# Kernel tuning notes

Hardware: AMD Instinct MI355X
Metric: run time of the kernel (lower is better)

The kernel has to match this reference:

```python
import jax, jax.numpy as jnp
import numpy as np

LK = 8  # db4 has 8 taps
LEVEL = 5
# pywt.Wavelet('db4').filter_bank[0] == dec_lo
DB4_LO = np.array([-0.010597401784997278, 0.032883011666982945, 0.030841381835986965,
                   -0.18703481171888114, -0.02798376941698385, 0.6308807679295904,
                   0.7148465705525415, 0.23037781330885523], dtype=np.float32)
DN = ('NCH', 'OIH', 'NCH')


def _wpt_kernels(level):
    # Filter_Free WPT: distinct kernel per child node; parent j even -> (lp, hp), odd -> (hp, lp)
    cmf = (-1.0) ** np.arange(LK)
    k_lp = DB4_LO
    k_hp = (DB4_LO[::-1] * cmf).astype(np.float32)
    ks = []
    for i in range(level):
        rows = []
        for j in range(2 ** i):
            rows += [k_lp, k_hp] if j % 2 == 0 else [k_hp, k_lp]
        ks.append(jnp.asarray(np.stack(rows)))  # [2^(i+1), LK]
    return ks


def setup_inputs() -> dict:
    key = jax.random.key(0)
    kx, kb = jax.random.split(key)
    B, N = 128, 32768
    inp = {'x': jax.random.normal(kx, (B, 1, N), dtype=jnp.float32)}
    for i, K in enumerate(_wpt_kernels(LEVEL)):
        inp[f'k{i + 1}'] = K
    for i in range(LEVEL):
        kb, sub = jax.random.split(kb)
        # small positive thresholds (Act_Init=0 would make the threshold an exact identity)
        inp[f'b{i + 1}'] = 0.1 * jax.random.uniform(sub, (2 ** (i + 1),), dtype=jnp.float32)
    return inp


def _analysis(c, K, b):
    # c: [B, G, M] parents -> [B, 2G, M//2] children; one grouped 8-tap conv for the whole level
    G = c.shape[1]
    cp = jnp.pad(c, ((0, 0), (0, 0), (LK // 2 - 1, LK // 2)))
    y = jax.lax.conv_general_dilated(cp, K[:, None, :], (2,), 'VALID',
                                     feature_group_count=G, dimension_numbers=DN)
    bb = b[None, :, None]
    # symmetric sigmoid soft-threshold (Thresh_SigSym), fused elementwise
    return y * (jax.nn.sigmoid(10.0 * (y - bb)) + jax.nn.sigmoid(-10.0 * (y + bb)))


def _synthesis(y, K):
    # adjoint of the strided analysis conv (conv_transpose): [B, 2G, M] -> [B, G, 2M]
    G = y.shape[1] // 2
    M = y.shape[2]
    W = jnp.flip(K, -1).reshape(G, 2, LK)  # sum the two children of each parent
    out = jax.lax.conv_general_dilated(y, W, (1,), [(LK - 1, LK - 1)], lhs_dilation=(2,),
                                       feature_group_count=G, dimension_numbers=DN)
    pl = LK // 2 - 1  # undo analysis left pad
    return out[:, :, pl:pl + 2 * M]


def reference(x, k1, k2, k3, k4, k5, b1, b2, b3, b4, b5):
    Ks = [k1, k2, k3, k4, k5]
    bs = [b1, b2, b3, b4, b5]
    c = x  # [B, 1, N]
    for K, b in zip(Ks, bs):
        c = _analysis(c, K, b)
    for K in Ks[::-1]:
        c = _synthesis(c, K)
    return c  # [B, 1, N] reconstruction
```

## Files before the change

### kernel.cpp

```cpp
#include <hip/hip_runtime.h>

#define TPB 256

constexpr int NSEQ = 32768;
constexpr int C0   = 2048;


__device__ __forceinline__ float gate(float y, float bb) {
    float e1 = __expf(-10.f * (y - bb));
    float e2 = __expf( 10.f * (y + bb));
    return __builtin_amdgcn_rcpf(1.f + e1) + __builtin_amdgcn_rcpf(1.f + e2);
}

template<int Sin, int Sout, int P, int Gout, int Nlev>
__device__ __forceinline__ void analysis_r4(
    const float* __restrict__ in, float* __restrict__ out,
    const float* __restrict__ kf, const float* __restrict__ bias, int outBase)
{
    constexpr int TPC = P / 4;
    constexpr int TOT = (Gout / 2) * TPC;
    for (int task = threadIdx.x; task < TOT; task += TPB) {
        const int c  = task / TPC;
        const int i0 = (task - c * TPC) * 4;

        float w[16];
        {
            const float4* ip = reinterpret_cast<const float4*>(in + c * Sin + 2 * i0);
            reinterpret_cast<float4*>(w)[0] = ip[0];
            reinterpret_cast<float4*>(w)[1] = ip[1];
            reinterpret_cast<float4*>(w)[2] = ip[2];
            reinterpret_cast<float4*>(w)[3] = ip[3];
        }
        float k0[8], k1[8];
        {
            const float4* kp = reinterpret_cast<const float4*>(kf + (2 * c) * 8);
            reinterpret_cast<float4*>(k0)[0] = kp[0];
            reinterpret_cast<float4*>(k0)[1] = kp[1];
            reinterpret_cast<float4*>(k1)[0] = kp[2];
            reinterpret_cast<float4*>(k1)[1] = kp[3];
        }
        const float b0 = bias[2 * c];
        const float b1 = bias[2 * c + 1];

        float o0[4], o1[4];
#pragma unroll
        for (int r = 0; r < 4; ++r) {
            float ya = 0.f, yb = 0.f;
#pragma unroll
            for (int t = 0; t < 8; ++t) {
                ya = fmaf(w[2 * r + t], k0[t], ya);
                yb = fmaf(w[2 * r + t], k1[t], yb);
            }
            const int m = outBase + i0 + r;
            const bool ok = ((unsigned)m < (unsigned)Nlev);
            o0[r] = ok ? ya * gate(ya, b0) : 0.f;
            o1[r] = ok ? yb * gate(yb, b1) : 0.f;
        }
        *reinterpret_cast<float4*>(out + (2 * c)     * Sout + i0) = *reinterpret_cast<float4*>(o0);
        *reinterpret_cast<float4*>(out + (2 * c + 1) * Sout + i0) = *reinterpret_cast<float4*>(o1);
    }
}

template<int Sin, int Sout, int P, int Gout, int Nlev>
__device__ __forceinline__ void synth_r8(
    const float* __restrict__ in, float* __restrict__ out,
    const float* __restrict__ kf, int outBase)
{
    constexpr int TPG = P / 8;
    constexpr int TOT = Gout * TPG;
    for (int task = threadIdx.x; task < TOT; task += TPB) {
        const int g   = task / TPG;
        const int nl0 = (task - g * TPG) * 8;

        float ya[8], yb[8];
        {
            const float4* p0 = reinterpret_cast<const float4*>(in + (2 * g) * Sin + nl0 / 2);
            const float4* p1 = reinterpret_cast<const float4*>(in + (2 * g + 1) * Sin + nl0 / 2);
            reinterpret_cast<float4*>(ya)[0] = p0[0];
            reinterpret_cast<float4*>(ya)[1] = p0[1];
            reinterpret_cast<float4*>(yb)[0] = p1[0];
            reinterpret_cast<float4*>(yb)[1] = p1[1];
        }
        float k0[8], k1[8];
        {
            const float4* kp = reinterpret_cast<const float4*>(kf + (2 * g) * 8);
            reinterpret_cast<float4*>(k0)[0] = kp[0];
            reinterpret_cast<float4*>(k0)[1] = kp[1];
            reinterpret_cast<float4*>(k1)[0] = kp[2];
            reinterpret_cast<float4*>(k1)[1] = kp[3];
        }

        float o[8];
#pragma unroll
        for (int r = 0; r < 8; ++r) {
            const int jr = (r + 1) >> 1;
            const int kb = 7 - (r & 1);
            float acc = 0.f;
#pragma unroll
            for (int q = 0; q < 4; ++q) {
                acc = fmaf(ya[jr + q], k0[kb - 2 * q], acc);
                acc = fmaf(yb[jr + q], k1[kb - 2 * q], acc);
            }
            const int m = outBase + nl0 + r;
            o[r] = ((unsigned)m < (unsigned)Nlev) ? acc : 0.f;
        }
        float* op = out + g * Sout + nl0;
        *reinterpret_cast<float4*>(op)     = *reinterpret_cast<float4*>(o);
        *reinterpret_cast<float4*>(op + 4) = *reinterpret_cast<float4*>(o + 4);
    }
}

__global__ __launch_bounds__(TPB) void wpt_fused(
    const float* __restrict__ x,
    const float* __restrict__ K1, const float* __restrict__ K2,
    const float* __restrict__ K3, const float* __restrict__ K4,
    const float* __restrict__ K5,
    const float* __restrict__ B1, const float* __restrict__ B2,
    const float* __restrict__ B3, const float* __restrict__ B4,
    const float* __restrict__ B5,
    float* __restrict__ out)
{
    __shared__ __align__(16) float bufA[2528];
    __shared__ __align__(16) float bufB[2512];
    __shared__ __align__(16) float kf[496];
    __shared__ float bss[62];

    const int tid   = threadIdx.x;
    const int batch = blockIdx.x >> 4;
    const int cid   = blockIdx.x & 15;
    const int s     = cid * C0;

    {
        const float* kin[5] = {K1, K2, K3, K4, K5};
        const float* bin[5] = {B1, B2, B3, B4, B5};
        const int koff[5] = {0, 16, 48, 112, 240};
        const int boff[5] = {0, 2, 6, 14, 30};
#pragma unroll
        for (int l = 0; l < 5; ++l) {
            for (int i = tid; i < (16 << l); i += TPB) kf[koff[l] + i] = kin[l][i];
            for (int i = tid; i < (2  << l); i += TPB) bss[boff[l] + i] = bin[l][i];
        }
    }

    {
        const float* xb = x + batch * NSEQ;
        const int base = s - 221;
        for (int i = tid; i < 2504; i += TPB) {
            const int g = base + i;
            bufA[i] = (i < 2490 && (unsigned)g < (unsigned)NSEQ) ? xb[g] : 0.f;
        }
    }
    __syncthreads();

    analysis_r4<2504, 1256, 1248,  2, 16384>(bufA, bufB, kf + 0,   bss + 0,  (s >> 1) - 109);
    __syncthreads();
    analysis_r4<1256,  632,  624,  4,  8192>(bufB, bufA, kf + 16,  bss + 2,  (s >> 2) - 53);
    __syncthreads();
    analysis_r4< 632,  312,  312,  8,  4096>(bufA, bufB, kf + 48,  bss + 6,  (s >> 3) - 25);
    __syncthreads();
    analysis_r4< 312,  152,  152, 16,  2048>(bufB, bufA, kf + 112, bss + 14, (s >> 4) - 11);
    __syncthreads();
    analysis_r4< 152,   72,   72, 32,  1024>(bufA, bufB, kf + 240, bss + 30, (s >> 5) - 4);
    __syncthreads();

    synth_r8<  72,  136,  136, 16,  2048>(bufB, bufA, kf + 240, (s >> 4) - 4);
    __syncthreads();
    synth_r8< 136,  264,  264,  8,  4096>(bufA, bufB, kf + 112, (s >> 3) - 4);
    __syncthreads();
    synth_r8< 264,  520,  520,  4,  8192>(bufB, bufA, kf + 48,  (s >> 2) - 4);
    __syncthreads();
    synth_r8< 520, 1032, 1032,  2, 16384>(bufA, bufB, kf + 16,  (s >> 1) - 4);
    __syncthreads();

    {
        float* ob = out + batch * NSEQ + s;
        const int i0 = tid * 8;
        float ya[12], yb[12];
        {
            const float4* p0 = reinterpret_cast<const float4*>(bufB + i0 / 2);
            const float4* p1 = reinterpret_cast<const float4*>(bufB + 1032 + i0 / 2);
            reinterpret_cast<float4*>(ya)[0] = p0[0];
            reinterpret_cast<float4*>(ya)[1] = p0[1];
            reinterpret_cast<float4*>(ya)[2] = p0[2];
            reinterpret_cast<float4*>(yb)[0] = p1[0];
            reinterpret_cast<float4*>(yb)[1] = p1[1];
            reinterpret_cast<float4*>(yb)[2] = p1[2];
        }
        float k0[8], k1[8];
        {
            const float4* kp = reinterpret_cast<const float4*>(kf);
            reinterpret_cast<float4*>(k0)[0] = kp[0];
            reinterpret_cast<float4*>(k0)[1] = kp[1];
            reinterpret_cast<float4*>(k1)[0] = kp[2];
            reinterpret_cast<float4*>(k1)[1] = kp[3];
        }
        float o[8];
#pragma unroll
        for (int r = 0; r < 8; ++r) {
            const int jr = ((r + 1) >> 1) + 2;
            const int kb = 7 - (r & 1);
            float acc = 0.f;
#pragma unroll
            for (int q = 0; q < 4; ++q) {
                acc = fmaf(ya[jr + q], k0[kb - 2 * q], acc);
                acc = fmaf(yb[jr + q], k1[kb - 2 * q], acc);
            }
            o[r] = acc;
        }
        *reinterpret_cast<float4*>(ob + i0)     = *reinterpret_cast<float4*>(o);
        *reinterpret_cast<float4*>(ob + i0 + 4) = *reinterpret_cast<float4*>(o + 4);
    }
}

extern "C" void kernel_launch(void* const* d_in, const int* in_sizes, int n_in,
                              void* d_out, int out_size, void* d_ws, size_t ws_size,
                              hipStream_t stream) {
    const int nbatch = in_sizes[0] / NSEQ;
    wpt_fused<<<dim3(nbatch * (NSEQ / C0)), dim3(TPB), 0, stream>>>(
        (const float*)d_in[0],
        (const float*)d_in[1], (const float*)d_in[2],
        (const float*)d_in[3], (const float*)d_in[4],
        (const float*)d_in[5],
        (const float*)d_in[6], (const float*)d_in[7],
        (const float*)d_in[8], (const float*)d_in[9],
        (const float*)d_in[10],
        (float*)d_out);
}
```

Measured before the change: 128.3 us.

## Store analysis-stage buffers in even/odd polyphase layout to avoid LDS bank conflicts

Analysis levels now keep each channel in LDS as separate even and odd sample planes, so a stride-2 decimating conv reads contiguous float4s, and outputs are written back already split into polyphase form for the next level. The input load deinterleaves x into even/odd halves. The final analysis level writes the natural layout that synthesis expects. The aim is to cut LDS bank conflicts and wide strided reads in the analysis loops, at the cost of float2 scattered stores and a strided global load.

Measured after the change: 122.5 us. 4.6% less time.

```diff
diff --git a/kernel.cpp b/kernel.cpp
--- a/kernel.cpp
+++ b/kernel.cpp
@@ -12,8 +12,8 @@
     return __builtin_amdgcn_rcpf(1.f + e1) + __builtin_amdgcn_rcpf(1.f + e2);
 }
 
-template<int Sin, int Sout, int P, int Gout, int Nlev>
-__device__ __forceinline__ void analysis_r4(
+template<int LEin, int LEout, int P, int Gout, int Nlev>
+__device__ __forceinline__ void analysis_pp(
     const float* __restrict__ in, float* __restrict__ out,
     const float* __restrict__ kf, const float* __restrict__ bias, int outBase)
 {
@@ -23,14 +23,14 @@
         const int c  = task / TPC;
         const int i0 = (task - c * TPC) * 4;
 
-        float w[16];
-        {
-            const float4* ip = reinterpret_cast<const float4*>(in + c * Sin + 2 * i0);
-            reinterpret_cast<float4*>(w)[0] = ip[0];
-            reinterpret_cast<float4*>(w)[1] = ip[1];
-            reinterpret_cast<float4*>(w)[2] = ip[2];
-            reinterpret_cast<float4*>(w)[3] = ip[3];
-        }
+        const float* ep = in + c * (2 * LEin) + i0;
+        const float* op = ep + LEin;
+        float e[8], o[8];
+        reinterpret_cast<float4*>(e)[0] = *reinterpret_cast<const float4*>(ep);
+        reinterpret_cast<float4*>(e)[1] = *reinterpret_cast<const float4*>(ep + 4);
+        reinterpret_cast<float4*>(o)[0] = *reinterpret_cast<const float4*>(op);
+        reinterpret_cast<float4*>(o)[1] = *reinterpret_cast<const float4*>(op + 4);
+
         float k0[8], k1[8];
         {
             const float4* kp = reinterpret_cast<const float4*>(kf + (2 * c) * 8);
@@ -42,22 +42,81 @@
         const float b0 = bias[2 * c];
         const float b1 = bias[2 * c + 1];
 
-        float o0[4], o1[4];
+        float v0[4], v1[4];
 #pragma unroll
         for (int r = 0; r < 4; ++r) {
             float ya = 0.f, yb = 0.f;
 #pragma unroll
-            for (int t = 0; t < 8; ++t) {
-                ya = fmaf(w[2 * r + t], k0[t], ya);
-                yb = fmaf(w[2 * r + t], k1[t], yb);
+            for (int u = 0; u < 4; ++u) {
+                ya = fmaf(e[r + u], k0[2 * u], ya);
+                ya = fmaf(o[r + u], k0[2 * u + 1], ya);
+                yb = fmaf(e[r + u], k1[2 * u], yb);
+                yb = fmaf(o[r + u], k1[2 * u + 1], yb);
             }
             const int m = outBase + i0 + r;
             const bool ok = ((unsigned)m < (unsigned)Nlev);
-            o0[r] = ok ? ya * gate(ya, b0) : 0.f;
-            o1[r] = ok ? yb * gate(yb, b1) : 0.f;
-        }
-        *reinterpret_cast<float4*>(out + (2 * c)     * Sout + i0) = *reinterpret_cast<float4*>(o0);
-        *reinterpret_cast<float4*>(out + (2 * c + 1) * Sout + i0) = *reinterpret_cast<float4*>(o1);
+            v0[r] = ok ? ya * gate(ya, b0) : 0.f;
+            v1[r] = ok ? yb * gate(yb, b1) : 0.f;
+        }
+
+        const int j0 = i0 >> 1;
+        float* ob0 = out + (2 * c) * (2 * LEout);
+        float* ob1 = ob0 + 2 * LEout;
+        *reinterpret_cast<float2*>(ob0 + j0)         = make_float2(v0[0], v0[2]);
+        *reinterpret_cast<float2*>(ob0 + LEout + j0) = make_float2(v0[1], v0[3]);
+        *reinterpret_cast<float2*>(ob1 + j0)         = make_float2(v1[0], v1[2]);
+        *reinterpret_cast<float2*>(ob1 + LEout + j0) = make_float2(v1[1], v1[3]);
+    }
+}
+
+template<int LEin, int Sout, int P, int Gout, int Nlev>
+__device__ __forceinline__ void analysis_pn(
+    const float* __restrict__ in, float* __restrict__ out,
+    const float* __restrict__ kf, const float* __restrict__ bias, int outBase)
+{
+    constexpr int TPC = P / 4;
+    constexpr int TOT = (Gout / 2) * TPC;
+    for (int task = threadIdx.x; task < TOT; task += TPB) {
+        const int c  = task / TPC;
+        const int i0 = (task - c * TPC) * 4;
+
+        const float* ep = in + c * (2 * LEin) + i0;
+        const float* op = ep + LEin;
+        float e[8], o[8];
+        reinterpret_cast<float4*>(e)[0] = *reinterpret_cast<const float4*>(ep);
+        reinterpret_cast<float4*>(e)[1] = *reinterpret_cast<const float4*>(ep + 4);
+        reinterpret_cast<float4*>(o)[0] = *reinterpret_cast<const float4*>(op);
+        reinterpret_cast<float4*>(o)[1] = *reinterpret_cast<const float4*>(op + 4);
+
+        float k0[8], k1[8];
+        {
+            const float4* kp = reinterpret_cast<const float4*>(kf + (2 * c) * 8);
+            reinterpret_cast<float4*>(k0)[0] = kp[0];
+            reinterpret_cast<float4*>(k0)[1] = kp[1];
+            reinterpret_cast<float4*>(k1)[0] = kp[2];
+            reinterpret_cast<float4*>(k1)[1] = kp[3];
+        }
+        const float b0 = bias[2 * c];
+        const float b1 = bias[2 * c + 1];
+
+        float v0[4], v1[4];
+#pragma unroll
+        for (int r = 0; r < 4; ++r) {
+            float ya = 0.f, yb = 0.f;
+#pragma unroll
+            for (int u = 0; u < 4; ++u) {
+                ya = fmaf(e[r + u], k0[2 * u], ya);
+                ya = fmaf(o[r + u], k0[2 * u + 1], ya);
+                yb = fmaf(e[r + u], k1[2 * u], yb);
+                yb = fmaf(o[r + u], k1[2 * u + 1], yb);
+            }
+            const int m = outBase + i0 + r;
+            const bool ok = ((unsigned)m < (unsigned)Nlev);
+            v0[r] = ok ? ya * gate(ya, b0) : 0.f;
+            v1[r] = ok ? yb * gate(yb, b1) : 0.f;
+        }
+        *reinterpret_cast<float4*>(out + (2 * c)     * Sout + i0) = *reinterpret_cast<float4*>(v0);
+        *reinterpret_cast<float4*>(out + (2 * c + 1) * Sout + i0) = *reinterpret_cast<float4*>(v1);
     }
 }
 
@@ -104,9 +163,9 @@
             const int m = outBase + nl0 + r;
             o[r] = ((unsigned)m < (unsigned)Nlev) ? acc : 0.f;
         }
-        float* op = out + g * Sout + nl0;
-        *reinterpret_cast<float4*>(op)     = *reinterpret_cast<float4*>(o);
-        *reinterpret_cast<float4*>(op + 4) = *reinterpret_cast<float4*>(o + 4);
+        float* opt = out + g * Sout + nl0;
+        *reinterpret_cast<float4*>(opt)     = *reinterpret_cast<float4*>(o);
+        *reinterpret_cast<float4*>(opt + 4) = *reinterpret_cast<float4*>(o + 4);
     }
 }
 
@@ -145,22 +204,25 @@
     {
         const float* xb = x + batch * NSEQ;
         const int base = s - 221;
-        for (int i = tid; i < 2504; i += TPB) {
-            const int g = base + i;
-            bufA[i] = (i < 2490 && (unsigned)g < (unsigned)NSEQ) ? xb[g] : 0.f;
-        }
-    }
-    __syncthreads();
-
-    analysis_r4<2504, 1256, 1248,  2, 16384>(bufA, bufB, kf + 0,   bss + 0,  (s >> 1) - 109);
-    __syncthreads();
-    analysis_r4<1256,  632,  624,  4,  8192>(bufB, bufA, kf + 16,  bss + 2,  (s >> 2) - 53);
-    __syncthreads();
-    analysis_r4< 632,  312,  312,  8,  4096>(bufA, bufB, kf + 48,  bss + 6,  (s >> 3) - 25);
-    __syncthreads();
-    analysis_r4< 312,  152,  152, 16,  2048>(bufB, bufA, kf + 112, bss + 14, (s >> 4) - 11);
-    __syncthreads();
-    analysis_r4< 152,   72,   72, 32,  1024>(bufA, bufB, kf + 240, bss + 30, (s >> 5) - 4);
+        for (int j = tid; j < 1252; j += TPB) {
+            const int g0 = base + 2 * j;
+            const int g1 = g0 + 1;
+            const bool okj = (j < 1245);
+            bufA[j]        = (okj && (unsigned)g0 < (unsigned)NSEQ) ? xb[g0] : 0.f;
+            bufA[1252 + j] = (okj && (unsigned)g1 < (unsigned)NSEQ) ? xb[g1] : 0.f;
+        }
+    }
+    __syncthreads();
+
+    analysis_pp<1252, 628, 1248,  2, 16384>(bufA, bufB, kf + 0,   bss + 0,  (s >> 1) - 109);
+    __syncthreads();
+    analysis_pp< 628, 316,  624,  4,  8192>(bufB, bufA, kf + 16,  bss + 2,  (s >> 2) - 53);
+    __syncthreads();
+    analysis_pp< 316, 156,  312,  8,  4096>(bufA, bufB, kf + 48,  bss + 6,  (s >> 3) - 25);
+    __syncthreads();
+    analysis_pp< 156,  76,  152, 16,  2048>(bufB, bufA, kf + 112, bss + 14, (s >> 4) - 11);
+    __syncthreads();
+    analysis_pn<  76,  72,   72, 32,  1024>(bufA, bufB, kf + 240, bss + 30, (s >> 5) - 4);
     __syncthreads();
 
     synth_r8<  72,  136,  136, 16,  2048>(bufB, bufA, kf + 240, (s >> 4) - 4);
```

## Store even/odd-deinterleaved shared buffers, double chunk size, specialize interior chunks

Applied to the files above, without the earlier changes.

Doubles the per-block chunk to 4096 samples, which halves the block count and shrinks the relative halo overhead. Each level's coefficients are now stored in shared memory split into even and odd phases, so analysis reads contiguous float4 vectors without stride-2 access and computes 8 outputs per thread. The sigmoid gate is rewritten with exp2 and a threshold pre-scaled on load, removing some multiplies. Interior chunks get a template path with no bounds checks. Costs are roughly double the shared memory per block and fewer blocks in flight, which may lower occupancy.

Result: faster. 123.5 us (-3.8%).

```diff
diff --git a/kernel.cpp b/kernel.cpp
--- a/kernel.cpp
+++ b/kernel.cpp
@@ -3,91 +3,120 @@
 #define TPB 256
 
 constexpr int NSEQ = 32768;
-constexpr int C0   = 2048;
-
-
-__device__ __forceinline__ float gate(float y, float bb) {
-    float e1 = __expf(-10.f * (y - bb));
-    float e2 = __expf( 10.f * (y + bb));
-    return __builtin_amdgcn_rcpf(1.f + e1) + __builtin_amdgcn_rcpf(1.f + e2);
-}
-
-template<int Sin, int Sout, int P, int Gout, int Nlev>
-__device__ __forceinline__ void analysis_r4(
+constexpr int C0   = 4096;
+constexpr float SCG = 14.4269504089f;
+
+
+__device__ __forceinline__ float4 ldf4(const float* p) { return *reinterpret_cast<const float4*>(p); }
+__device__ __forceinline__ void   stf4(float* p, const float4 v) { *reinterpret_cast<float4*>(p) = v; }
+
+__device__ __forceinline__ float gated(float y, float tb) {
+    float e1 = __builtin_amdgcn_exp2f(fmaf(y, -SCG, tb));
+    float e2 = __builtin_amdgcn_exp2f(fmaf(y,  SCG, tb));
+    return y * (__builtin_amdgcn_rcpf(1.f + e1) + __builtin_amdgcn_rcpf(1.f + e2));
+}
+
+template<int LEin, int LEout, int P, int PAIRS, int Nlev, int BOFF, bool EDGE, bool LAST>
+__device__ __forceinline__ void analysis8(
     const float* __restrict__ in, float* __restrict__ out,
     const float* __restrict__ kf, const float* __restrict__ bias, int outBase)
 {
-    constexpr int TPC = P / 4;
-    constexpr int TOT = (Gout / 2) * TPC;
+    constexpr int TPC = P / 8;
+    constexpr int TOT = PAIRS * TPC;
     for (int task = threadIdx.x; task < TOT; task += TPB) {
         const int c  = task / TPC;
-        const int i0 = (task - c * TPC) * 4;
-
-        float w[16];
-        {
-            const float4* ip = reinterpret_cast<const float4*>(in + c * Sin + 2 * i0);
-            reinterpret_cast<float4*>(w)[0] = ip[0];
-            reinterpret_cast<float4*>(w)[1] = ip[1];
-            reinterpret_cast<float4*>(w)[2] = ip[2];
-            reinterpret_cast<float4*>(w)[3] = ip[3];
-        }
+        const int i0 = (task - c * TPC) * 8;
+
+        const float* pe = in + c * (2 * LEin);
+        const float* pa = BOFF ? (pe + LEin) : pe;
+        const float* pb = BOFF ? pe : (pe + LEin);
+
+        float a[12], b[12];
+        reinterpret_cast<float4*>(a)[0] = ldf4(pa + i0);
+        reinterpret_cast<float4*>(a)[1] = ldf4(pa + i0 + 4);
+        reinterpret_cast<float4*>(a)[2] = ldf4(pa + i0 + 8);
+        reinterpret_cast<float4*>(b)[0] = ldf4(pb + i0);
+        reinterpret_cast<float4*>(b)[1] = ldf4(pb + i0 + 4);
+        reinterpret_cast<float4*>(b)[2] = ldf4(pb + i0 + 8);
+
         float k0[8], k1[8];
         {
-            const float4* kp = reinterpret_cast<const float4*>(kf + (2 * c) * 8);
-            reinterpret_cast<float4*>(k0)[0] = kp[0];
-            reinterpret_cast<float4*>(k0)[1] = kp[1];
-            reinterpret_cast<float4*>(k1)[0] = kp[2];
-            reinterpret_cast<float4*>(k1)[1] = kp[3];
-        }
-        const float b0 = bias[2 * c];
-        const float b1 = bias[2 * c + 1];
-
-        float o0[4], o1[4];
-#pragma unroll
-        for (int r = 0; r < 4; ++r) {
+            const float* kp = kf + (2 * c) * 8;
+            reinterpret_cast<float4*>(k0)[0] = ldf4(kp);
+            reinterpret_cast<float4*>(k0)[1] = ldf4(kp + 4);
+            reinterpret_cast<float4*>(k1)[0] = ldf4(kp + 8);
+            reinterpret_cast<float4*>(k1)[1] = ldf4(kp + 12);
+        }
+        const float tb0 = bias[2 * c];
+        const float tb1 = bias[2 * c + 1];
+
+        float v0[8], v1[8];
+#pragma unroll
+        for (int r = 0; r < 8; ++r) {
             float ya = 0.f, yb = 0.f;
 #pragma unroll
-            for (int t = 0; t < 8; ++t) {
-                ya = fmaf(w[2 * r + t], k0[t], ya);
-                yb = fmaf(w[2 * r + t], k1[t], yb);
-            }
-            const int m = outBase + i0 + r;
-            const bool ok = ((unsigned)m < (unsigned)Nlev);
-            o0[r] = ok ? ya * gate(ya, b0) : 0.f;
-            o1[r] = ok ? yb * gate(yb, b1) : 0.f;
-        }
-        *reinterpret_cast<float4*>(out + (2 * c)     * Sout + i0) = *reinterpret_cast<float4*>(o0);
-        *reinterpret_cast<float4*>(out + (2 * c + 1) * Sout + i0) = *reinterpret_cast<float4*>(o1);
-    }
-}
-
-template<int Sin, int Sout, int P, int Gout, int Nlev>
-__device__ __forceinline__ void synth_r8(
+            for (int u = 0; u < 4; ++u) {
+                ya = fmaf(a[r + u], k0[2 * u], ya);
+                ya = fmaf(b[r + BOFF + u], k0[2 * u + 1], ya);
+                yb = fmaf(a[r + u], k1[2 * u], yb);
+                yb = fmaf(b[r + BOFF + u], k1[2 * u + 1], yb);
+            }
+            float w0 = gated(ya, tb0);
+            float w1 = gated(yb, tb1);
+            if (EDGE) {
+                const bool ok = ((unsigned)(outBase + i0 + r) < (unsigned)Nlev);
+                w0 = ok ? w0 : 0.f;
+                w1 = ok ? w1 : 0.f;
+            }
+            v0[r] = w0; v1[r] = w1;
+        }
+
+        if (LAST) {
+            float* o0 = out + (2 * c) * LEout + i0;
+            float* o1 = out + (2 * c + 1) * LEout + i0;
+            stf4(o0,     make_float4(v0[0], v0[1], v0[2], v0[3]));
+            stf4(o0 + 4, make_float4(v0[4], v0[5], v0[6], v0[7]));
+            stf4(o1,     make_float4(v1[0], v1[1], v1[2], v1[3]));
+            stf4(o1 + 4, make_float4(v1[4], v1[5], v1[6], v1[7]));
+        } else {
+            const int j0 = i0 >> 1;
+            float* ob0 = out + (2 * c) * (2 * LEout);
+            float* ob1 = ob0 + 2 * LEout;
+            stf4(ob0 + j0,         make_float4(v0[0], v0[2], v0[4], v0[6]));
+            stf4(ob0 + LEout + j0, make_float4(v0[1], v0[3], v0[5], v0[7]));
+            stf4(ob1 + j0,         make_float4(v1[0], v1[2], v1[4], v1[6]));
+            stf4(ob1 + LEout + j0, make_float4(v1[1], v1[3], v1[5], v1[7]));
+        }
+    }
+}
+
+template<int Sin, int Sout, int P, int G, int Nlev, bool EDGE>
+__device__ __forceinline__ void synth8(
     const float* __restrict__ in, float* __restrict__ out,
     const float* __restrict__ kf, int outBase)
 {
     constexpr int TPG = P / 8;
-    constexpr int TOT = Gout * TPG;
+    constexpr int TOT = G * TPG;
     for (int task = threadIdx.x; task < TOT; task += TPB) {
         const int g   = task / TPG;
         const int nl0 = (task - g * TPG) * 8;
 
         float ya[8], yb[8];
         {
-            const float4* p0 = reinterpret_cast<const float4*>(in + (2 * g) * Sin + nl0 / 2);
-            const float4* p1 = reinterpret_cast<const float4*>(in + (2 * g + 1) * Sin + nl0 / 2);
-            reinterpret_cast<float4*>(ya)[0] = p0[0];
-            reinterpret_cast<float4*>(ya)[1] = p0[1];
-            reinterpret_cast<float4*>(yb)[0] = p1[0];
-            reinterpret_cast<float4*>(yb)[1] = p1[1];
+            const float* p0 = in + (2 * g) * Sin + nl0 / 2;
+            const float* p1 = p0 + Sin;
+            reinterpret_cast<float4*>(ya)[0] = ldf4(p0);
+            reinterpret_cast<float4*>(ya)[1] = ldf4(p0 + 4);
+            reinterpret_cast<float4*>(yb)[0] = ldf4(p1);
+            reinterpret_cast<float4*>(yb)[1] = ldf4(p1 + 4);
         }
         float k0[8], k1[8];
         {
-            const float4* kp = reinterpret_cast<const float4*>(kf + (2 * g) * 8);
-            reinterpret_cast<float4*>(k0)[0] = kp[0];
-            reinterpret_cast<float4*>(k0)[1] = kp[1];
-            reinterpret_cast<float4*>(k1)[0] = kp[2];
-            reinterpret_cast<float4*>(k1)[1] = kp[3];
+            const float* kp = kf + (2 * g) * 8;
+            reinterpret_cast<float4*>(k0)[0] = ldf4(kp);
+            reinterpret_cast<float4*>(k0)[1] = ldf4(kp + 4);
+            reinterpret_cast<float4*>(k1)[0] = ldf4(kp + 8);
+            reinterpret_cast<float4*>(k1)[1] = ldf4(kp + 12);
         }
 
         float o[8];
@@ -101,12 +130,104 @@
                 acc = fmaf(ya[jr + q], k0[kb - 2 * q], acc);
                 acc = fmaf(yb[jr + q], k1[kb - 2 * q], acc);
             }
-            const int m = outBase + nl0 + r;
-            o[r] = ((unsigned)m < (unsigned)Nlev) ? acc : 0.f;
+            if (EDGE) {
+                const bool ok = ((unsigned)(outBase + nl0 + r) < (unsigned)Nlev);
+                acc = ok ? acc : 0.f;
+            }
+            o[r] = acc;
         }
         float* op = out + g * Sout + nl0;
-        *reinterpret_cast<float4*>(op)     = *reinterpret_cast<float4*>(o);
-        *reinterpret_cast<float4*>(op + 4) = *reinterpret_cast<float4*>(o + 4);
+        stf4(op,     make_float4(o[0], o[1], o[2], o[3]));
+        stf4(op + 4, make_float4(o[4], o[5], o[6], o[7]));
+    }
+}
+
+template<bool EDGE>
+__device__ __forceinline__ void run_chunk(
+    const float* __restrict__ xb, float* __restrict__ ob, int s,
+    float* __restrict__ bufA, float* __restrict__ bufB,
+    const float* __restrict__ kf, const float* __restrict__ bss)
+{
+    const int tid = threadIdx.x;
+
+    {
+        const int b0 = s - 222;
+        if (EDGE) {
+            for (int t = tid; t < 1138; t += TPB) {
+                const int g = b0 + 4 * t;
+                const float e0 = ((unsigned)g       < (unsigned)NSEQ) ? xb[g]     : 0.f;
+                const float o0 = ((unsigned)(g + 1) < (unsigned)NSEQ) ? xb[g + 1] : 0.f;
+                const float e1 = ((unsigned)(g + 2) < (unsigned)NSEQ) ? xb[g + 2] : 0.f;
+                const float o1 = ((unsigned)(g + 3) < (unsigned)NSEQ) ? xb[g + 3] : 0.f;
+                *reinterpret_cast<float2*>(bufA + 2 * t)        = make_float2(e0, e1);
+                *reinterpret_cast<float2*>(bufA + 2276 + 2 * t) = make_float2(o0, o1);
+            }
+        } else {
+            for (int t = tid; t < 1138; t += TPB) {
+                const float* p = xb + b0 + 4 * t;
+                const float2 fa = *reinterpret_cast<const float2*>(p);
+                const float2 fb = *reinterpret_cast<const float2*>(p + 2);
+                *reinterpret_cast<float2*>(bufA + 2 * t)        = make_float2(fa.x, fb.x);
+                *reinterpret_cast<float2*>(bufA + 2276 + 2 * t) = make_float2(fa.y, fb.y);
+            }
+        }
+    }
+    __syncthreads();
+
+    analysis8<2276, 1140, 2272,  1, 16384, 1, EDGE, false>(bufA, bufB, kf + 0,   bss + 0,  (s >> 1) - 109);
+    __syncthreads();
+    analysis8<1140,  572, 1136,  2,  8192, 0, EDGE, false>(bufB, bufA, kf + 16,  bss + 2,  (s >> 2) - 53);
+    __syncthreads();
+    analysis8< 572,  284,  568,  4,  4096, 0, EDGE, false>(bufA, bufB, kf + 48,  bss + 6,  (s >> 3) - 25);
+    __syncthreads();
+    analysis8< 284,  140,  280,  8,  2048, 0, EDGE, false>(bufB, bufA, kf + 112, bss + 14, (s >> 4) - 11);
+    __syncthreads();
+    analysis8< 140,  136,  136, 16,  1024, 0, EDGE, true >(bufA, bufB, kf + 240, bss + 30, (s >> 5) - 4);
+    __syncthreads();
+
+    synth8< 136,  264,  264, 16,  2048, EDGE>(bufB, bufA, kf + 240, (s >> 4) - 4);
+    __syncthreads();
+    synth8< 264,  520,  520,  8,  4096, EDGE>(bufA, bufB, kf + 112, (s >> 3) - 4);
+    __syncthreads();
+    synth8< 520, 1032, 1032,  4,  8192, EDGE>(bufB, bufA, kf + 48,  (s >> 2) - 4);
+    __syncthreads();
+    synth8<1032, 2056, 2056,  2, 16384, EDGE>(bufA, bufB, kf + 16,  (s >> 1) - 4);
+    __syncthreads();
+
+    for (int task = tid; task < 512; task += TPB) {
+        const int i0 = task * 8;
+        float ya[12], yb[12];
+        {
+            const float* p0 = bufB + i0 / 2;
+            const float* p1 = p0 + 2056;
+            reinterpret_cast<float4*>(ya)[0] = ldf4(p0);
+            reinterpret_cast<float4*>(ya)[1] = ldf4(p0 + 4);
+            reinterpret_cast<float4*>(ya)[2] = ldf4(p0 + 8);
+            reinterpret_cast<float4*>(yb)[0] = ldf4(p1);
+            reinterpret_cast<float4*>(yb)[1] = ldf4(p1 + 4);
+            reinterpret_cast<float4*>(yb)[2] = ldf4(p1 + 8);
+        }
+        float k0[8], k1[8];
+        reinterpret_cast<float4*>(k0)[0] = ldf4(kf);
+        reinterpret_cast<float4*>(k0)[1] = ldf4(kf + 4);
+        reinterpret_cast<float4*>(k1)[0] = ldf4(kf + 8);
+        reinterpret_cast<float4*>(k1)[1] = ldf4(kf + 12);
+
+        float o[8];
+#pragma unroll
+        for (int r = 0; r < 8; ++r) {
+            const int jr = ((r + 1) >> 1) + 2;
+            const int kb = 7 - (r & 1);
+            float acc = 0.f;
+#pragma unroll
+            for (int q = 0; q < 4; ++q) {
+                acc = fmaf(ya[jr + q], k0[kb - 2 * q], acc);
+                acc = fmaf(yb[jr + q], k1[kb - 2 * q], acc);
+            }
+            o[r] = acc;
+        }
+        stf4(ob + i0,     make_float4(o[0], o[1], o[2], o[3]));
+        stf4(ob + i0 + 4, make_float4(o[4], o[5], o[6], o[7]));
     }
 }
 
@@ -120,14 +241,14 @@
     const float* __restrict__ B5,
     float* __restrict__ out)
 {
-    __shared__ __align__(16) float bufA[2528];
-    __shared__ __align__(16) float bufB[2512];
+    __shared__ __align__(16) float bufA[4576];
+    __shared__ __align__(16) float bufB[4560];
     __shared__ __align__(16) float kf[496];
     __shared__ float bss[62];
 
     const int tid   = threadIdx.x;
-    const int batch = blockIdx.x >> 4;
-    const int cid   = blockIdx.x & 15;
+    const int batch = blockIdx.x >> 3;
+    const int cid   = blockIdx.x & 7;
     const int s     = cid * C0;
 
     {
@@ -138,78 +259,17 @@
 #pragma unroll
         for (int l = 0; l < 5; ++l) {
             for (int i = tid; i < (16 << l); i += TPB) kf[koff[l] + i] = kin[l][i];
-            for (int i = tid; i < (2  << l); i += TPB) bss[boff[l] + i] = bin[l][i];
-        }
-    }
-
-    {
-        const float* xb = x + batch * NSEQ;
-        const int base = s - 221;
-        for (int i = tid; i < 2504; i += TPB) {
-            const int g = base + i;
-            bufA[i] = (i < 2490 && (unsigned)g < (unsigned)NSEQ) ? xb[g] : 0.f;
-        }
-    }
-    __syncthreads();
-
-    analysis_r4<2504, 1256, 1248,  2, 16384>(bufA, bufB, kf + 0,   bss + 0,  (s >> 1) - 109);
-    __syncthreads();
-    analysis_r4<1256,  632,  624,  4,  8192>(bufB, bufA, kf + 16,  bss + 2,  (s >> 2) - 53);
-    __syncthreads();
-    analysis_r4< 632,  312,  312,  8,  4096>(bufA, bufB, kf + 48,  bss + 6,  (s >> 3) - 25);
-    __syncthreads();
-    analysis_r4< 312,  152,  152, 16,  2048>(bufB, bufA, kf + 112, bss + 14, (s >> 4) - 11);
-    __syncthreads();
-    analysis_r4< 152,   72,   72, 32,  1024>(bufA, bufB, kf + 240, bss + 30, (s >> 5) - 4);
-    __syncthreads();
-
-    synth_r8<  72,  136,  136, 16,  2048>(bufB, bufA, kf + 240, (s >> 4) - 4);
-    __syncthreads();
-    synth_r8< 136,  264,  264,  8,  4096>(bufA, bufB, kf + 112, (s >> 3) - 4);
-    __syncthreads();
-    synth_r8< 264,  520,  520,  4,  8192>(bufB, bufA, kf + 48,  (s >> 2) - 4);
-    __syncthreads();
-    synth_r8< 520, 1032, 1032,  2, 16384>(bufA, bufB, kf + 16,  (s >> 1) - 4);
-    __syncthreads();
-
-    {
-        float* ob = out + batch * NSEQ + s;
-        const int i0 = tid * 8;
-        float ya[12], yb[12];
-        {
-            const float4* p0 = reinterpret_cast<const float4*>(bufB + i0 / 2);
-            const float4* p1 = reinterpret_cast<const float4*>(bufB + 1032 + i0 / 2);
-            reinterpret_cast<float4*>(ya)[0] = p0[0];
-            reinterpret_cast<float4*>(ya)[1] = p0[1];
-            reinterpret_cast<float4*>(ya)[2] = p0[2];
-            reinterpret_cast<float4*>(yb)[0] = p1[0];
-            reinterpret_cast<float4*>(yb)[1] = p1[1];
-            reinterpret_cast<float4*>(yb)[2] = p1[2];
-        }
-        float k0[8], k1[8];
-        {
-            const float4* kp = reinterpret_cast<const float4*>(kf);
-            reinterpret_cast<float4*>(k0)[0] = kp[0];
-            reinterpret_cast<float4*>(k0)[1] = kp[1];
-            reinterpret_cast<float4*>(k1)[0] = kp[2];
-            reinterpret_cast<float4*>(k1)[1] = kp[3];
-        }
-        float o[8];
-#pragma unroll
-        for (int r = 0; r < 8; ++r) {
-            const int jr = ((r + 1) >> 1) + 2;
-            const int kb = 7 - (r & 1);
-            float acc = 0.f;
-#pragma unroll
-            for (int q = 0; q < 4; ++q) {
-                acc = fmaf(ya[jr + q], k0[kb - 2 * q], acc);
-                acc = fmaf(yb[jr + q], k1[kb - 2 * q], acc);
-            }
-            o[r] = acc;
-        }
-        *reinterpret_cast<float4*>(ob + i0)     = *reinterpret_cast<float4*>(o);
-        *reinterpret_cast<float4*>(ob + i0 + 4) = *reinterpret_cast<float4*>(o + 4);
-    }
+            for (int i = tid; i < (2  << l); i += TPB) bss[boff[l] + i] = SCG * bin[l][i];
+        }
+    }
+
+    const float* xb = x + batch * NSEQ;
+    float* ob = out + batch * NSEQ + s;
+
+    if (cid == 0 || cid == 7)
+        run_chunk<true >(xb, ob, s, bufA, bufB, kf, bss);
+    else
+        run_chunk<false>(xb, ob, s, bufA, bufB, kf, bss);
 }
 
 extern "C" void kernel_launch(void* const* d_in, const int* in_sizes, int n_in,
```
